# Kernel optimization log

Hardware: AMD Instinct MI355X
Metric: run time of the kernel (lower is better)

Reference implementation:

```python
import jax, jax.numpy as jnp
import numpy as np

SHIFT = 1  # fixed shift_direction for determinism


def setup_inputs() -> dict:
    key = jax.random.key(0)
    k1, k2, k3 = jax.random.split(key, 3)
    x = jax.random.normal(k1, (1, 256, 28, 28), dtype=jnp.float32)
    w1 = jax.random.normal(k2, (8, 64, 3), dtype=jnp.float32)
    w2 = jax.random.normal(k3, (32, 4, 3), dtype=jnp.float32)
    return {"x": x, "w1": w1, "w2": w2}


def reference(x, w1, w2):
    # x: (1, 256, 28, 28) -> (64, 4, 28, 28); roll along H (axis 2 here == torch axis 3)
    t = x.reshape(64, 4, 28, 28)
    t = jnp.roll(t, SHIFT, axis=2)
    # unfold over H, kernel 3, pad 1: tap j at output row m reads padded row m+j
    p = jnp.pad(t, ((0, 0), (0, 0), (1, 1), (0, 0)))
    taps = jnp.stack([p[:, :, j:j + 28, :] for j in range(3)], axis=2)  # (64,4,3,28,28)
    # grouped conv over H: mix 64 input channels -> 8 output channels, per group o=4
    t4 = jnp.einsum('iojmn,kij->komn', taps, w1)  # (8,4,28,28)
    # unfold over W, kernel 3, pad 1
    p2 = jnp.pad(t4, ((0, 0), (0, 0), (0, 0), (1, 1)))
    taps2 = jnp.stack([p2[:, :, :, k:k + 28] for k in range(3)], axis=3)  # (8,4,28,3,28)
    # grouped conv over W: mix 4 groups -> 32 channels, per group o=8
    t6 = jnp.einsum('ojmkn,ijk->iomn', taps2, w2)  # (32,8,28,28)
    return t6.reshape(1, 256, 28, 28)
```

## Files before the change

### kernel.cpp

```cpp
#include <hip/hip_runtime.h>

__global__ __launch_bounds__(256) void conv1_kernel(const float* __restrict__ x,
                                                    const float* __restrict__ w1,
                                                    float* __restrict__ t4) {
    const int k = blockIdx.y;
    __shared__ float w1s[192];
    if (threadIdx.x < 192) w1s[threadIdx.x] = w1[k * 192 + threadIdx.x];
    __syncthreads();

    const int idx = blockIdx.x * 256 + threadIdx.x;
    if (idx >= 4 * 28 * 28) return;
    const int n = idx % 28;
    const int m = (idx / 28) % 28;
    const int o = idx / 784;

    float acc = 0.f;
#pragma unroll
    for (int j = 0; j < 3; ++j) {
        const int mj = m + j;
        if (mj == 0 || mj == 29) continue;
        int hh = mj - 2;
        if (hh < 0) hh += 28;
        const float* xp = x + o * 784 + hh * 28 + n;
#pragma unroll 8
        for (int i = 0; i < 64; ++i) {
            acc = fmaf(w1s[i * 3 + j], xp[i * 4 * 784], acc);
        }
    }
    t4[k * 3136 + idx] = acc;
}

__global__ __launch_bounds__(256) void conv2_kernel(const float* __restrict__ t4,
                                                    const float* __restrict__ w2,
                                                    float* __restrict__ out) {
    const int i = blockIdx.y;
    __shared__ float w2s[12];
    if (threadIdx.x < 12) w2s[threadIdx.x] = w2[i * 12 + threadIdx.x];
    __syncthreads();

    const int idx = blockIdx.x * 256 + threadIdx.x;
    if (idx >= 8 * 28 * 28) return;
    const int n = idx % 28;
    const int om = idx / 28;
    const int m = om % 28;
    const int o = om / 28;

    const float* tp = t4 + o * 3136 + m * 28;
    float acc = 0.f;
#pragma unroll
    for (int j = 0; j < 4; ++j) {
#pragma unroll
        for (int k = 0; k < 3; ++k) {
            const int nn = n + k - 1;
            if (nn < 0 || nn >= 28) continue;
            acc = fmaf(w2s[j * 3 + k], tp[j * 784 + nn], acc);
        }
    }
    out[i * 6272 + idx] = acc;
}

extern "C" void kernel_launch(void* const* d_in, const int* in_sizes, int n_in,
                              void* d_out, int out_size, void* d_ws, size_t ws_size,
                              hipStream_t stream) {
    const float* x  = (const float*)d_in[0];
    const float* w1 = (const float*)d_in[1];
    const float* w2 = (const float*)d_in[2];
    float* out = (float*)d_out;
    float* t4  = (float*)d_ws;

    conv1_kernel<<<dim3(13, 8),  256, 0, stream>>>(x,  w1, t4);
    conv2_kernel<<<dim3(25, 32), 256, 0, stream>>>(t4, w2, out);
}
```

Baseline: 67.44 us.

## Fuse both grouped convolutions into one per-row kernel with shared-memory intermediate

Replaces the two kernels with one kernel launched per output row m. Each block computes the 32x28 slice of the intermediate t4 for that row into padded shared memory using float4 loads of x, then runs the W-direction conv from shared memory and writes float4 outputs. This removes the second launch and the global round-trip of t4. The cost is only 28 blocks, which leaves most of the GPU idle, and each thread now runs a longer serial loop.

```diff
diff --git a/kernel.cpp b/kernel.cpp
--- a/kernel.cpp
+++ b/kernel.cpp
@@ -1,62 +1,82 @@
 #include <hip/hip_runtime.h>
 
-__global__ __launch_bounds__(256) void conv1_kernel(const float* __restrict__ x,
-                                                    const float* __restrict__ w1,
-                                                    float* __restrict__ t4) {
-    const int k = blockIdx.y;
-    __shared__ float w1s[192];
-    if (threadIdx.x < 192) w1s[threadIdx.x] = w1[k * 192 + threadIdx.x];
+__global__ __launch_bounds__(256) void fused_shiftconv(const float* __restrict__ x,
+                                                       const float* __restrict__ w1,
+                                                       const float* __restrict__ w2,
+                                                       float* __restrict__ out) {
+    __shared__ float w1s[8 * 193];
+    __shared__ float w2s[384];
+    __shared__ float t4s[32 * 33];
+
+    const int tid = threadIdx.x;
+    const int m = blockIdx.x;
+
+    for (int idx = tid; idx < 1536; idx += 256) {
+        const int k = idx / 192;
+        w1s[k * 193 + (idx - k * 192)] = w1[idx];
+    }
+    if (tid < 128) {
+        w2s[tid] = w2[tid];
+        w2s[tid + 128] = w2[tid + 128];
+        w2s[tid + 256] = w2[tid + 256];
+    }
+    if (tid < 64) {
+        t4s[(tid & 31) * 33 + (tid >> 5) * 29] = 0.f;
+    }
     __syncthreads();
 
-    const int idx = blockIdx.x * 256 + threadIdx.x;
-    if (idx >= 4 * 28 * 28) return;
-    const int n = idx % 28;
-    const int m = (idx / 28) % 28;
-    const int o = idx / 784;
-
-    float acc = 0.f;
+    if (tid < 224) {
+        const int o = tid / 56;
+        const int q = (tid >> 3) % 7;
+        const int k = tid & 7;
+        const float* wk = &w1s[k * 193];
+        float4 acc = make_float4(0.f, 0.f, 0.f, 0.f);
 #pragma unroll
-    for (int j = 0; j < 3; ++j) {
-        const int mj = m + j;
-        if (mj == 0 || mj == 29) continue;
-        int hh = mj - 2;
-        if (hh < 0) hh += 28;
-        const float* xp = x + o * 784 + hh * 28 + n;
+        for (int j = 0; j < 3; ++j) {
+            const int mj = m + j;
+            if (mj == 0 || mj == 29) continue;
+            int hh = mj - 2;
+            if (hh < 0) hh += 28;
+            const float* xb = x + o * 784 + hh * 28 + q * 4;
 #pragma unroll 8
-        for (int i = 0; i < 64; ++i) {
-            acc = fmaf(w1s[i * 3 + j], xp[i * 4 * 784], acc);
+            for (int i = 0; i < 64; ++i) {
+                const float4 v = *reinterpret_cast<const float4*>(xb + i * 3136);
+                const float w = wk[i * 3 + j];
+                acc.x = fmaf(w, v.x, acc.x);
+                acc.y = fmaf(w, v.y, acc.y);
+                acc.z = fmaf(w, v.z, acc.z);
+                acc.w = fmaf(w, v.w, acc.w);
+            }
         }
+        float* dst = &t4s[(k * 4 + o) * 33 + 1 + q * 4];
+        dst[0] = acc.x; dst[1] = acc.y; dst[2] = acc.z; dst[3] = acc.w;
     }
-    t4[k * 3136 + idx] = acc;
-}
-
-__global__ __launch_bounds__(256) void conv2_kernel(const float* __restrict__ t4,
-                                                    const float* __restrict__ w2,
-                                                    float* __restrict__ out) {
-    const int i = blockIdx.y;
-    __shared__ float w2s[12];
-    if (threadIdx.x < 12) w2s[threadIdx.x] = w2[i * 12 + threadIdx.x];
     __syncthreads();
 
-    const int idx = blockIdx.x * 256 + threadIdx.x;
-    if (idx >= 8 * 28 * 28) return;
-    const int n = idx % 28;
-    const int om = idx / 28;
-    const int m = om % 28;
-    const int o = om / 28;
-
-    const float* tp = t4 + o * 3136 + m * 28;
-    float acc = 0.f;
+    const int i2 = tid >> 3;
+    const int o2 = tid & 7;
+    const float* wr = &w2s[i2 * 12];
+    float* orow = out + (i2 * 8 + o2) * 784 + m * 28;
 #pragma unroll
-    for (int j = 0; j < 4; ++j) {
+    for (int q = 0; q < 7; ++q) {
+        float4 r;
+        float* rp = &r.x;
 #pragma unroll
-        for (int k = 0; k < 3; ++k) {
-            const int nn = n + k - 1;
-            if (nn < 0 || nn >= 28) continue;
-            acc = fmaf(w2s[j * 3 + k], tp[j * 784 + nn], acc);
+        for (int e = 0; e < 4; ++e) {
+            const int n = q * 4 + e;
+            float acc = 0.f;
+#pragma unroll
+            for (int j = 0; j < 4; ++j) {
+                const float* trow = &t4s[(o2 * 4 + j) * 33 + n];
+#pragma unroll
+                for (int kk = 0; kk < 3; ++kk) {
+                    acc = fmaf(wr[j * 3 + kk], trow[kk], acc);
+                }
+            }
+            rp[e] = acc;
         }
+        *reinterpret_cast<float4*>(orow + q * 4) = r;
     }
-    out[i * 6272 + idx] = acc;
 }
 
 extern "C" void kernel_launch(void* const* d_in, const int* in_sizes, int n_in,
@@ -66,8 +86,6 @@
     const float* w1 = (const float*)d_in[1];
     const float* w2 = (const float*)d_in[2];
     float* out = (float*)d_out;
-    float* t4  = (float*)d_ws;
 
-    conv1_kernel<<<dim3(13, 8),  256, 0, stream>>>(x,  w1, t4);
-    conv2_kernel<<<dim3(25, 32), 256, 0, stream>>>(t4, w2, out);
+    fused_shiftconv<<<dim3(28), 256, 0, stream>>>(x, w1, w2, out);
 }
```

New measurement: 72.69 us. 1.08x slower.
